# Performance work log

Measured on AMD Instinct MI355X. Metric: run time of the kernel, lower is better.

Reference implementation:

```python
import jax, jax.numpy as jnp
import numpy as np

N_GRAPHS = 256
STEPS = 3


def setup_inputs() -> dict:
    key = jax.random.key(0)
    ks = jax.random.split(key, 8)
    N, d, out = 100000, 512, 256
    s = 0.05
    x = jax.random.normal(ks[0], (N, d), dtype=jnp.float32)
    batch = jnp.sort(jax.random.randint(ks[1], (N,), 0, N_GRAPHS)).astype(jnp.int64)
    W_ih = jax.random.normal(ks[2], (4 * d, 2 * d), dtype=jnp.float32) * s
    W_hh = jax.random.normal(ks[3], (4 * d, d), dtype=jnp.float32) * s
    b_ih = jax.random.normal(ks[4], (4 * d,), dtype=jnp.float32) * s
    b_hh = jax.random.normal(ks[5], (4 * d,), dtype=jnp.float32) * s
    W_proj = jax.random.normal(ks[6], (out, 2 * d), dtype=jnp.float32) * s
    b_proj = jax.random.normal(ks[7], (out,), dtype=jnp.float32) * s
    return {"x": x, "batch": batch, "W_ih": W_ih, "W_hh": W_hh,
            "b_ih": b_ih, "b_hh": b_hh, "W_proj": W_proj, "b_proj": b_proj}


def _set2set(x, batch, W_ih, W_hh, b_ih, b_hh):
    N, d = x.shape
    B = N_GRAPHS
    h = jnp.zeros((B, d), x.dtype)
    c = jnp.zeros((B, d), x.dtype)
    q_star = jnp.zeros((B, 2 * d), x.dtype)
    for _ in range(STEPS):
        # single-step LSTM cell (PyTorch gate order i,f,g,o)
        gates = q_star @ W_ih.T + b_ih + h @ W_hh.T + b_hh
        i, f, g, o = jnp.split(gates, 4, axis=-1)
        c = jax.nn.sigmoid(f) * c + jax.nn.sigmoid(i) * jnp.tanh(g)
        h = jax.nn.sigmoid(o) * jnp.tanh(c)
        q = h                                   # [B, d]
        # segment softmax attention over nodes
        e = jnp.sum(x * q[batch], axis=-1)      # [N]
        m = jax.ops.segment_max(e, batch, num_segments=B)
        m = jnp.where(jnp.isfinite(m), m, 0.0)  # guard empty segments
        ex = jnp.exp(e - m[batch])
        denom = jax.ops.segment_sum(ex, batch, num_segments=B) + 1e-16
        a = ex / denom[batch]                   # [N]
        r = jax.ops.segment_sum(a[:, None] * x, batch, num_segments=B)  # [B, d]
        q_star = jnp.concatenate([q, r], axis=-1)
    return q_star


def reference(x, batch, W_ih, W_hh, b_ih, b_hh, W_proj, b_proj):
    pooled = _set2set(x, batch, W_ih, W_hh, b_ih, b_hh)  # [B, 2d]
    return pooled @ W_proj.T + b_proj                    # [B, out]
```

## Files before the change

kernel.cpp:

```cpp
#include <hip/hip_runtime.h>
#include <hip/hip_bf16.h>


typedef __bf16 bf16_t;
typedef __bf16 bf16x8 __attribute__((ext_vector_type(8)));
typedef float  f32x4  __attribute__((ext_vector_type(4)));

#define D     512
#define B_GR  256
#define FOURD 2048
#define KCAT  1536
#define AWAVES 16
#define DET_BLOCKS 400

__device__ __forceinline__ float load_f(const void* b, int i, int f32) {
    return f32 ? ((const float*)b)[i] : (float)((const bf16_t*)b)[i];
}

__global__ void detect_part1(const int* __restrict__ b32, int N,
                             const unsigned short* __restrict__ xh,
                             int* __restrict__ partA, int* __restrict__ partB) {
    __shared__ int sA, sB;
    if (threadIdx.x == 0) { sA = 0; sB = 0; }
    __syncthreads();
    int gid = blockIdx.x * blockDim.x + threadIdx.x;
    int stride = gridDim.x * blockDim.x;
    int dec = 0;
    for (int i = gid; i < N - 1; i += stride)
        if (b32[i] > b32[i + 1]) dec = 1;
    int bad = 0;
    for (int i = gid; i < 1024; i += stride) {
        unsigned e = (xh[i] >> 7) & 0xff;
        if (e >= 134) bad = 1;
    }
    if (dec) atomicOr(&sA, 1);
    if (bad) atomicOr(&sB, 1);
    __syncthreads();
    if (threadIdx.x == 0) { partA[blockIdx.x] = sA; partB[blockIdx.x] = sB; }
}

__global__ void detect_part2(const int* __restrict__ partA,
                             const int* __restrict__ partB, int nblk,
                             int* __restrict__ flags) {
    __shared__ int sA, sB;
    if (threadIdx.x == 0) { sA = 0; sB = 0; }
    __syncthreads();
    int a = 0, b = 0;
    for (int i = threadIdx.x; i < nblk; i += blockDim.x) {
        a |= partA[i];
        b |= partB[i];
    }
    if (a) atomicOr(&sA, 1);
    if (b) atomicOr(&sB, 1);
    __syncthreads();
    if (threadIdx.x == 0) { flags[0] = sA; flags[1] = sB; }
}

__global__ void seg_bounds_kernel(const void* __restrict__ batch, int N, int B,
                                  const int* __restrict__ flags,
                                  int* __restrict__ seg) {
    int n = blockIdx.x * blockDim.x + threadIdx.x;
    if (n >= N) return;
    const int is64 = flags[0];
    const int* b32 = (const int*)batch;
    const long long* b64 = (const long long*)batch;
    int cur = is64 ? (int)b64[n] : b32[n];
    if (n == 0) {
        for (int b = 0; b <= cur && b <= B; ++b) seg[b] = 0;
    } else {
        int prev = is64 ? (int)b64[n - 1] : b32[n - 1];
        for (int b = prev + 1; b <= cur && b <= B; ++b) seg[b] = n;
    }
    if (n == N - 1) {
        for (int b = cur + 1; b <= B; ++b) seg[b] = N;
    }
}

#define WCAT_E (FOURD * KCAT)
#define WP_E   (256 * 1024)
__global__ void prep_kernel(const void* __restrict__ W_ih,
                            const void* __restrict__ W_hh,
                            const void* __restrict__ b_ih,
                            const void* __restrict__ b_hh,
                            const void* __restrict__ W_proj,
                            const void* __restrict__ b_proj,
                            const int* __restrict__ flags,
                            bf16_t* __restrict__ Wcat, bf16_t* __restrict__ Wp,
                            float* __restrict__ bsum, float* __restrict__ bp) {
    const int f32 = flags[1];
    int gid = blockIdx.x * blockDim.x + threadIdx.x;
    int stride = gridDim.x * blockDim.x;
    const int total = WCAT_E + WP_E + FOURD + 256;
    for (int idx = gid; idx < total; idx += stride) {
        if (idx < WCAT_E) {
            int r = idx / KCAT, k = idx - r * KCAT;
            float v = (k < 1024) ? load_f(W_ih, r * 1024 + k, f32)
                                 : load_f(W_hh, r * 512 + (k - 1024), f32);
            Wcat[idx] = (bf16_t)v;
        } else if (idx < WCAT_E + WP_E) {
            int j = idx - WCAT_E;
            Wp[j] = (bf16_t)load_f(W_proj, j, f32);
        } else if (idx < WCAT_E + WP_E + FOURD) {
            int i = idx - WCAT_E - WP_E;
            bsum[i] = load_f(b_ih, i, f32) + load_f(b_hh, i, f32);
        } else {
            int i = idx - WCAT_E - WP_E - FOURD;
            bp[i] = load_f(b_proj, i, f32);
        }
    }
}

__global__ void lstm0_kernel(const float* __restrict__ bsum,
                             float* __restrict__ c, float* __restrict__ h,
                             bf16_t* __restrict__ Abuf) {
    int idx = blockIdx.x * blockDim.x + threadIdx.x;
    int b = idx >> 9, t = idx & 511;
    float gi = bsum[t], gf = bsum[512 + t], gg = bsum[1024 + t], go = bsum[1536 + t];
    (void)gf;
    float si = 1.f / (1.f + __expf(-gi));
    float so = 1.f / (1.f + __expf(-go));
    float tg = tanhf(gg);
    float cn = si * tg;
    float hn = so * tanhf(cn);
    c[idx] = cn;
    h[idx] = hn;
    bf16_t hb = (bf16_t)hn;
    Abuf[(size_t)b * KCAT + t]        = hb;
    Abuf[(size_t)b * KCAT + 1024 + t] = hb;
}

__global__ __launch_bounds__(64)
void gemm_lstm(const bf16_t* __restrict__ AbufIn,
               const bf16_t* __restrict__ Wcat,
               const float* __restrict__ bsum,
               float* __restrict__ c, float* __restrict__ h,
               bf16_t* __restrict__ AbufOut) {
    const int lane  = threadIdx.x;
    const int t0    = blockIdx.x * 16;
    const int m0    = blockIdx.y * 16;
    const int rowA  = m0 + (lane & 15);
    const int colB  = t0 + (lane & 15);
    const int kbase = (lane >> 4) * 8;

    f32x4 acc[4] = {{0,0,0,0},{0,0,0,0},{0,0,0,0},{0,0,0,0}};

    for (int k0 = 0; k0 < KCAT; k0 += 32) {
        int k = k0 + kbase;
        bf16x8 a = *(const bf16x8*)(AbufIn + (size_t)rowA * KCAT + k);
#pragma unroll
        for (int g = 0; g < 4; ++g) {
            bf16x8 bfr = *(const bf16x8*)(Wcat + (size_t)(g * 512 + colB) * KCAT + k);
            acc[g] = __builtin_amdgcn_mfma_f32_16x16x32_bf16(a, bfr, acc[g], 0, 0, 0);
        }
    }

    const int col   = colB;
    const int rbase = (lane >> 4) * 4;
    float bi = bsum[col], bf = bsum[512 + col], bg = bsum[1024 + col], bo = bsum[1536 + col];
#pragma unroll
    for (int r = 0; r < 4; ++r) {
        int m = m0 + rbase + r;
        float gi = acc[0][r] + bi;
        float gf = acc[1][r] + bf;
        float gg = acc[2][r] + bg;
        float go = acc[3][r] + bo;
        size_t ci = (size_t)m * D + col;
        float cv = c[ci];
        float si = 1.f / (1.f + __expf(-gi));
        float sf = 1.f / (1.f + __expf(-gf));
        float so = 1.f / (1.f + __expf(-go));
        float tg = tanhf(gg);
        float cn = sf * cv + si * tg;
        float hn = so * tanhf(cn);
        c[ci] = cn;
        h[ci] = hn;
        bf16_t hb = (bf16_t)hn;
        AbufOut[(size_t)m * KCAT + col]        = hb;
        AbufOut[(size_t)m * KCAT + 1024 + col] = hb;
    }
}


template<bool WRXB>
__device__ __forceinline__ void scan_f32(const float* __restrict__ xp,
                                         bf16_t* __restrict__ xb,
                                         int s, int cnt, int wave, int lane,
                                         const float* hl,
                                         float& m_w, float& s_w, float* r_w) {
    int i = 4 * wave;
    for (; i + 4 <= cnt; i += 4 * AWAVES) {
        size_t off = (((size_t)(s + i)) << 9) + (size_t)(lane * 8);
        float xr[4][8];
#pragma unroll
        for (int r = 0; r < 4; ++r) {
            const float* p = xp + off + (size_t)r * D;
            float4 v0 = *(const float4*)p;
            float4 v1 = *(const float4*)(p + 4);
            xr[r][0] = v0.x; xr[r][1] = v0.y; xr[r][2] = v0.z; xr[r][3] = v0.w;
            xr[r][4] = v1.x; xr[r][5] = v1.y; xr[r][6] = v1.z; xr[r][7] = v1.w;
        }
        if (WRXB) {
#pragma unroll
            for (int r = 0; r < 4; ++r) {
                bf16x8 v;
#pragma unroll
                for (int j = 0; j < 8; ++j) v[j] = (bf16_t)xr[r][j];
                *(bf16x8*)(xb + off + (size_t)r * D) = v;
            }
        }
        float d[4] = {0.f, 0.f, 0.f, 0.f};
#pragma unroll
        for (int j = 0; j < 8; ++j) {
#pragma unroll
            for (int r = 0; r < 4; ++r) d[r] += xr[r][j] * hl[j];
        }
#pragma unroll
        for (int o = 32; o > 0; o >>= 1) {
#pragma unroll
            for (int r = 0; r < 4; ++r) d[r] += __shfl_xor(d[r], o, 64);
        }
        float mx    = fmaxf(fmaxf(d[0], d[1]), fmaxf(d[2], d[3]));
        float m_new = fmaxf(m_w, mx);
        float alpha = __expf(m_w - m_new);
        float p0 = __expf(d[0] - m_new), p1 = __expf(d[1] - m_new);
        float p2 = __expf(d[2] - m_new), p3 = __expf(d[3] - m_new);
        s_w = s_w * alpha + ((p0 + p1) + (p2 + p3));
#pragma unroll
        for (int j = 0; j < 8; ++j)
            r_w[j] = r_w[j] * alpha + p0 * xr[0][j] + p1 * xr[1][j]
                                    + p2 * xr[2][j] + p3 * xr[3][j];
        m_w = m_new;
    }
    if (i < cnt) {
        int rem = cnt - i;
        size_t off = (((size_t)(s + i)) << 9) + (size_t)(lane * 8);
        float xr[4][8];
#pragma unroll
        for (int r = 0; r < 4; ++r) {
            if (r < rem) {
                const float* p = xp + off + (size_t)r * D;
                float4 v0 = *(const float4*)p;
                float4 v1 = *(const float4*)(p + 4);
                xr[r][0] = v0.x; xr[r][1] = v0.y; xr[r][2] = v0.z; xr[r][3] = v0.w;
                xr[r][4] = v1.x; xr[r][5] = v1.y; xr[r][6] = v1.z; xr[r][7] = v1.w;
            } else {
#pragma unroll
                for (int j = 0; j < 8; ++j) xr[r][j] = 0.f;
            }
        }
        if (WRXB) {
#pragma unroll
            for (int r = 0; r < 4; ++r) {
                if (r < rem) {
                    bf16x8 v;
#pragma unroll
                    for (int j = 0; j < 8; ++j) v[j] = (bf16_t)xr[r][j];
                    *(bf16x8*)(xb + off + (size_t)r * D) = v;
                }
            }
        }
        float d[4] = {0.f, 0.f, 0.f, 0.f};
#pragma unroll
        for (int j = 0; j < 8; ++j) {
#pragma unroll
            for (int r = 0; r < 4; ++r) d[r] += xr[r][j] * hl[j];
        }
#pragma unroll
        for (int o = 32; o > 0; o >>= 1) {
#pragma unroll
            for (int r = 0; r < 4; ++r) d[r] += __shfl_xor(d[r], o, 64);
        }
#pragma unroll
        for (int r = 0; r < 4; ++r)
            if (r >= rem) d[r] = -INFINITY;
        float mx    = fmaxf(fmaxf(d[0], d[1]), fmaxf(d[2], d[3]));
        float m_new = fmaxf(m_w, mx);
        float alpha = __expf(m_w - m_new);
        float p0 = __expf(d[0] - m_new), p1 = __expf(d[1] - m_new);
        float p2 = __expf(d[2] - m_new), p3 = __expf(d[3] - m_new);
        s_w = s_w * alpha + ((p0 + p1) + (p2 + p3));
#pragma unroll
        for (int j = 0; j < 8; ++j)
            r_w[j] = r_w[j] * alpha + p0 * xr[0][j] + p1 * xr[1][j]
                                    + p2 * xr[2][j] + p3 * xr[3][j];
        m_w = m_new;
    }
}

__device__ __forceinline__ void scan_bf16(const bf16_t* __restrict__ xp,
                                          int s, int cnt, int wave, int lane,
                                          const float* hl,
                                          float& m_w, float& s_w, float* r_w) {
    int i = 4 * wave;
    for (; i + 4 <= cnt; i += 4 * AWAVES) {
        size_t off = (((size_t)(s + i)) << 9) + (size_t)(lane * 8);
        float xr[4][8];
#pragma unroll
        for (int r = 0; r < 4; ++r) {
            bf16x8 v = *(const bf16x8*)(xp + off + (size_t)r * D);
#pragma unroll
            for (int j = 0; j < 8; ++j) xr[r][j] = (float)v[j];
        }
        float d[4] = {0.f, 0.f, 0.f, 0.f};
#pragma unroll
        for (int j = 0; j < 8; ++j) {
#pragma unroll
            for (int r = 0; r < 4; ++r) d[r] += xr[r][j] * hl[j];
        }
#pragma unroll
        for (int o = 32; o > 0; o >>= 1) {
#pragma unroll
            for (int r = 0; r < 4; ++r) d[r] += __shfl_xor(d[r], o, 64);
        }
        float mx    = fmaxf(fmaxf(d[0], d[1]), fmaxf(d[2], d[3]));
        float m_new = fmaxf(m_w, mx);
        float alpha = __expf(m_w - m_new);
        float p0 = __expf(d[0] - m_new), p1 = __expf(d[1] - m_new);
        float p2 = __expf(d[2] - m_new), p3 = __expf(d[3] - m_new);
        s_w = s_w * alpha + ((p0 + p1) + (p2 + p3));
#pragma unroll
        for (int j = 0; j < 8; ++j)
            r_w[j] = r_w[j] * alpha + p0 * xr[0][j] + p1 * xr[1][j]
                                    + p2 * xr[2][j] + p3 * xr[3][j];
        m_w = m_new;
    }
    if (i < cnt) {
        int rem = cnt - i;
        size_t off = (((size_t)(s + i)) << 9) + (size_t)(lane * 8);
        float xr[4][8];
#pragma unroll
        for (int r = 0; r < 4; ++r) {
            if (r < rem) {
                bf16x8 v = *(const bf16x8*)(xp + off + (size_t)r * D);
#pragma unroll
                for (int j = 0; j < 8; ++j) xr[r][j] = (float)v[j];
            } else {
#pragma unroll
                for (int j = 0; j < 8; ++j) xr[r][j] = 0.f;
            }
        }
        float d[4] = {0.f, 0.f, 0.f, 0.f};
#pragma unroll
        for (int j = 0; j < 8; ++j) {
#pragma unroll
            for (int r = 0; r < 4; ++r) d[r] += xr[r][j] * hl[j];
        }
#pragma unroll
        for (int o = 32; o > 0; o >>= 1) {
#pragma unroll
            for (int r = 0; r < 4; ++r) d[r] += __shfl_xor(d[r], o, 64);
        }
#pragma unroll
        for (int r = 0; r < 4; ++r)
            if (r >= rem) d[r] = -INFINITY;
        float mx    = fmaxf(fmaxf(d[0], d[1]), fmaxf(d[2], d[3]));
        float m_new = fmaxf(m_w, mx);
        float alpha = __expf(m_w - m_new);
        float p0 = __expf(d[0] - m_new), p1 = __expf(d[1] - m_new);
        float p2 = __expf(d[2] - m_new), p3 = __expf(d[3] - m_new);
        s_w = s_w * alpha + ((p0 + p1) + (p2 + p3));
#pragma unroll
        for (int j = 0; j < 8; ++j)
            r_w[j] = r_w[j] * alpha + p0 * xr[0][j] + p1 * xr[1][j]
                                    + p2 * xr[2][j] + p3 * xr[3][j];
        m_w = m_new;
    }
}

template<int STEP0, int USE_XB>
__global__ __launch_bounds__(1024)
void attention_kernel(const void* __restrict__ x, bf16_t* __restrict__ xb,
                      int N, const int* __restrict__ seg,
                      const float* __restrict__ hbuf,
                      bf16_t* __restrict__ AbufOut,
                      const int* __restrict__ flags) {
    __shared__ float racc2[AWAVES][D];
    __shared__ float red_m[AWAVES], red_s[AWAVES];

    const int f32x = flags[1];

    const int b = blockIdx.x;
    int s  = seg[b];
    int en = seg[b + 1];
    s  = (s  < 0) ? 0 : ((s  > N) ? N : s);
    en = (en < s) ? s : ((en > N) ? N : en);
    const int cnt  = en - s;
    const int tid  = threadIdx.x;
    const int wave = tid >> 6;
    const int lane = tid & 63;

    float hl[8];
    {
        const float* hp = hbuf + ((size_t)b << 9) + lane * 8;
#pragma unroll
        for (int j = 0; j < 8; ++j) hl[j] = hp[j];
    }

    float m_w = -INFINITY, s_w = 0.f;
    float r_w[8];
#pragma unroll
    for (int j = 0; j < 8; ++j) r_w[j] = 0.f;

    if (f32x) {
        if (STEP0 || !USE_XB) {
            scan_f32<(STEP0 && USE_XB)>((const float*)x, xb, s, cnt,
                                        wave, lane, hl, m_w, s_w, r_w);
        } else {
            scan_bf16(xb, s, cnt, wave, lane, hl, m_w, s_w, r_w);
        }
    } else {
        scan_bf16((const bf16_t*)x, s, cnt, wave, lane, hl, m_w, s_w, r_w);
    }

    if (lane == 0) { red_m[wave] = m_w; red_s[wave] = s_w; }
    __syncthreads();

    float M = -INFINITY, S = 0.f;
#pragma unroll
    for (int w = 0; w < AWAVES; ++w)
        if (red_s[w] > 0.f) M = fmaxf(M, red_m[w]);
#pragma unroll
    for (int w = 0; w < AWAVES; ++w)
        if (red_s[w] > 0.f) S += red_s[w] * __expf(red_m[w] - M);
    float Sinv  = 1.f / (S + 1e-16f);
    float scale = (s_w > 0.f) ? __expf(m_w - M) * Sinv : 0.f;

#pragma unroll
    for (int j = 0; j < 8; ++j) racc2[wave][lane * 8 + j] = r_w[j] * scale;
    __syncthreads();

    if (tid < D) {
        float r = 0.f;
#pragma unroll
        for (int w = 0; w < AWAVES; ++w) r += racc2[w][tid];
        AbufOut[(size_t)b * KCAT + 512 + tid] = (bf16_t)r;
    }
}

__global__ __launch_bounds__(64)
void gemm_proj(const bf16_t* __restrict__ A,
               const bf16_t* __restrict__ Wp, const float* __restrict__ bp,
               void* __restrict__ out, const int* __restrict__ flags) {
    const int f32o  = flags[1];
    const int lane  = threadIdx.x;
    const int n0    = blockIdx.x * 16;
    const int m0    = blockIdx.y * 16;
    const int rowA  = m0 + (lane & 15);
    const int rowB  = n0 + (lane & 15);
    const int kbase = (lane >> 4) * 8;

    f32x4 acc = {0.f, 0.f, 0.f, 0.f};
    for (int k0 = 0; k0 < 1024; k0 += 32) {
        int k = k0 + kbase;
        bf16x8 a = *(const bf16x8*)(A  + (size_t)rowA * KCAT + k);
        bf16x8 b = *(const bf16x8*)(Wp + (size_t)rowB * 1024 + k);
        acc = __builtin_amdgcn_mfma_f32_16x16x32_bf16(a, b, acc, 0, 0, 0);
    }
    const int col   = n0 + (lane & 15);
    const int rbase = (lane >> 4) * 4;
    float bias = bp[col];
#pragma unroll
    for (int r = 0; r < 4; ++r) {
        int m = m0 + rbase + r;
        float v = acc[r] + bias;
        if (f32o) ((float*)out)[(size_t)m * 256 + col]  = v;
        else      ((bf16_t*)out)[(size_t)m * 256 + col] = (bf16_t)v;
    }
}

extern "C" void kernel_launch(void* const* d_in, const int* in_sizes, int n_in,
                              void* d_out, int out_size, void* d_ws, size_t ws_size,
                              hipStream_t stream) {
    const void* x      = d_in[0];
    const void* batch  = d_in[1];
    const void* W_ih   = d_in[2];
    const void* W_hh   = d_in[3];
    const void* b_ih   = d_in[4];
    const void* b_hh   = d_in[5];
    const void* W_proj = d_in[6];
    const void* b_proj = d_in[7];

    const int N = in_sizes[1];
    const int B = B_GR;

    char* p = (char*)d_ws;
    size_t used = 0;
    auto carve = [&](size_t bytes) {
        void* r = (void*)p;
        size_t a = (bytes + 1023) & ~(size_t)1023;
        p += a;
        used += a;
        return r;
    };
    float*  c_buf = (float*)carve((size_t)B * D * 4);
    float*  h_buf = (float*)carve((size_t)B * D * 4);
    bf16_t* Abuf0 = (bf16_t*)carve((size_t)B * KCAT * 2);
    bf16_t* Abuf1 = (bf16_t*)carve((size_t)B * KCAT * 2);
    bf16_t* Wcat  = (bf16_t*)carve((size_t)FOURD * KCAT * 2);
    bf16_t* Wp    = (bf16_t*)carve((size_t)256 * 1024 * 2);
    float*  bsum  = (float*)carve((size_t)FOURD * 4);
    float*  bp    = (float*)carve((size_t)256 * 4);
    int*    seg   = (int*)carve((size_t)(B + 1) * 4);
    int*    flags = (int*)carve(8);
    int*    partA = (int*)carve(DET_BLOCKS * 4);
    int*    partB = (int*)carve(DET_BLOCKS * 4);
    if (used > ws_size) return;
    bf16_t* xb = (bf16_t*)carve((size_t)N * D * 2);
    int use_xb = (used <= ws_size) ? 1 : 0;

    detect_part1<<<DET_BLOCKS, 256, 0, stream>>>(
        (const int*)batch, N, (const unsigned short*)x, partA, partB);
    detect_part2<<<1, 512, 0, stream>>>(partA, partB, DET_BLOCKS, flags);
    seg_bounds_kernel<<<(N + 255) / 256, 256, 0, stream>>>(batch, N, B, flags, seg);
    prep_kernel<<<1024, 256, 0, stream>>>(W_ih, W_hh, b_ih, b_hh, W_proj, b_proj,
                                          flags, Wcat, Wp, bsum, bp);

    lstm0_kernel<<<(B * D) / 256, 256, 0, stream>>>(bsum, c_buf, h_buf, Abuf0);
    if (use_xb)
        attention_kernel<1, 1><<<B, 1024, 0, stream>>>(x, xb, N, seg,
                                                       h_buf, Abuf0, flags);
    else
        attention_kernel<1, 0><<<B, 1024, 0, stream>>>(x, xb, N, seg,
                                                       h_buf, Abuf0, flags);

    gemm_lstm<<<dim3(D / 16, B / 16), 64, 0, stream>>>(
        Abuf0, Wcat, bsum, c_buf, h_buf, Abuf1);
    if (use_xb)
        attention_kernel<0, 1><<<B, 1024, 0, stream>>>(x, xb, N, seg,
                                                       h_buf, Abuf1, flags);
    else
        attention_kernel<0, 0><<<B, 1024, 0, stream>>>(x, xb, N, seg,
                                                       h_buf, Abuf1, flags);
    gemm_lstm<<<dim3(D / 16, B / 16), 64, 0, stream>>>(
        Abuf1, Wcat, bsum, c_buf, h_buf, Abuf0);
    if (use_xb)
        attention_kernel<0, 1><<<B, 1024, 0, stream>>>(x, xb, N, seg,
                                                       h_buf, Abuf0, flags);
    else
        attention_kernel<0, 0><<<B, 1024, 0, stream>>>(x, xb, N, seg,
                                                       h_buf, Abuf0, flags);

    gemm_proj<<<dim3(256 / 16, B / 16), 64, 0, stream>>>(Abuf0, Wp, bp, d_out, flags);
}
```

Baseline: 421.0 us.

## Fuse seg bounds into prep, lstm0 into first attention, projection into last attention

Folds segment-boundary computation into the weight-prep kernel, computes the step-0 LSTM state inline inside the first attention kernel, and fuses the final projection GEMM into the last attention kernel as a per-graph scalar dot product. This removes three kernel launches and their global round-trips. The fused projection uses scalar FMAs over bf16 weights instead of MFMA, and each block rereads the whole projection matrix. The step-0 h/c values are no longer written to h_buf, and gemm_lstm is assumed to depend only on c_buf and Abuf.

Result: slower. 443.0 us (+5.2%).

```diff
diff --git a/kernel.cpp b/kernel.cpp
--- a/kernel.cpp
+++ b/kernel.cpp
@@ -56,40 +56,40 @@
     if (threadIdx.x == 0) { flags[0] = sA; flags[1] = sB; }
 }
 
-__global__ void seg_bounds_kernel(const void* __restrict__ batch, int N, int B,
-                                  const int* __restrict__ flags,
-                                  int* __restrict__ seg) {
-    int n = blockIdx.x * blockDim.x + threadIdx.x;
-    if (n >= N) return;
-    const int is64 = flags[0];
-    const int* b32 = (const int*)batch;
-    const long long* b64 = (const long long*)batch;
-    int cur = is64 ? (int)b64[n] : b32[n];
-    if (n == 0) {
-        for (int b = 0; b <= cur && b <= B; ++b) seg[b] = 0;
-    } else {
-        int prev = is64 ? (int)b64[n - 1] : b32[n - 1];
-        for (int b = prev + 1; b <= cur && b <= B; ++b) seg[b] = n;
-    }
-    if (n == N - 1) {
-        for (int b = cur + 1; b <= B; ++b) seg[b] = N;
-    }
-}
-
 #define WCAT_E (FOURD * KCAT)
 #define WP_E   (256 * 1024)
-__global__ void prep_kernel(const void* __restrict__ W_ih,
-                            const void* __restrict__ W_hh,
-                            const void* __restrict__ b_ih,
-                            const void* __restrict__ b_hh,
-                            const void* __restrict__ W_proj,
-                            const void* __restrict__ b_proj,
-                            const int* __restrict__ flags,
-                            bf16_t* __restrict__ Wcat, bf16_t* __restrict__ Wp,
-                            float* __restrict__ bsum, float* __restrict__ bp) {
+__global__ void prep_seg_kernel(const void* __restrict__ W_ih,
+                                const void* __restrict__ W_hh,
+                                const void* __restrict__ b_ih,
+                                const void* __restrict__ b_hh,
+                                const void* __restrict__ W_proj,
+                                const void* __restrict__ b_proj,
+                                const void* __restrict__ batch, int N, int B,
+                                const int* __restrict__ flags,
+                                bf16_t* __restrict__ Wcat, bf16_t* __restrict__ Wp,
+                                float* __restrict__ bsum, float* __restrict__ bp,
+                                int* __restrict__ seg) {
     const int f32 = flags[1];
     int gid = blockIdx.x * blockDim.x + threadIdx.x;
     int stride = gridDim.x * blockDim.x;
+
+    if (gid < N) {
+        const int n = gid;
+        const int is64 = flags[0];
+        const int* b32 = (const int*)batch;
+        const long long* b64 = (const long long*)batch;
+        int cur = is64 ? (int)b64[n] : b32[n];
+        if (n == 0) {
+            for (int b = 0; b <= cur && b <= B; ++b) seg[b] = 0;
+        } else {
+            int prev = is64 ? (int)b64[n - 1] : b32[n - 1];
+            for (int b = prev + 1; b <= cur && b <= B; ++b) seg[b] = n;
+        }
+        if (n == N - 1) {
+            for (int b = cur + 1; b <= B; ++b) seg[b] = N;
+        }
+    }
+
     const int total = WCAT_E + WP_E + FOURD + 256;
     for (int idx = gid; idx < total; idx += stride) {
         if (idx < WCAT_E) {
@@ -110,23 +110,14 @@
     }
 }
 
-__global__ void lstm0_kernel(const float* __restrict__ bsum,
-                             float* __restrict__ c, float* __restrict__ h,
-                             bf16_t* __restrict__ Abuf) {
-    int idx = blockIdx.x * blockDim.x + threadIdx.x;
-    int b = idx >> 9, t = idx & 511;
-    float gi = bsum[t], gf = bsum[512 + t], gg = bsum[1024 + t], go = bsum[1536 + t];
-    (void)gf;
+__device__ __forceinline__ void lstm0_math(const float* __restrict__ bsum,
+                                           int t, float& cn, float& hn) {
+    float gi = bsum[t], gg = bsum[1024 + t], go = bsum[1536 + t];
     float si = 1.f / (1.f + __expf(-gi));
     float so = 1.f / (1.f + __expf(-go));
     float tg = tanhf(gg);
-    float cn = si * tg;
-    float hn = so * tanhf(cn);
-    c[idx] = cn;
-    h[idx] = hn;
-    bf16_t hb = (bf16_t)hn;
-    Abuf[(size_t)b * KCAT + t]        = hb;
-    Abuf[(size_t)b * KCAT + 1024 + t] = hb;
+    cn = si * tg;
+    hn = so * tanhf(cn);
 }
 
 __global__ __launch_bounds__(64)
@@ -367,15 +358,22 @@
     }
 }
 
-template<int STEP0, int USE_XB>
+template<int STEP0, int USE_XB, int PROJ>
 __global__ __launch_bounds__(1024)
 void attention_kernel(const void* __restrict__ x, bf16_t* __restrict__ xb,
                       int N, const int* __restrict__ seg,
                       const float* __restrict__ hbuf,
+                      const float* __restrict__ bsum,
+                      float* __restrict__ c_buf,
                       bf16_t* __restrict__ AbufOut,
+                      const bf16_t* __restrict__ Wp,
+                      const float* __restrict__ bp,
+                      void* __restrict__ out,
                       const int* __restrict__ flags) {
     __shared__ float racc2[AWAVES][D];
     __shared__ float red_m[AWAVES], red_s[AWAVES];
+    __shared__ __align__(16) bf16_t qsb[PROJ ? 1024 : 1];
+    __shared__ float pout[PROJ ? 4 : 1][PROJ ? 256 : 1];
 
     const int f32x = flags[1];
 
@@ -390,7 +388,14 @@
     const int lane = tid & 63;
 
     float hl[8];
-    {
+    if (STEP0) {
+#pragma unroll
+        for (int j = 0; j < 8; ++j) {
+            float cn, hn;
+            lstm0_math(bsum, lane * 8 + j, cn, hn);
+            hl[j] = hn;
+        }
+    } else {
         const float* hp = hbuf + ((size_t)b << 9) + lane * 8;
 #pragma unroll
         for (int j = 0; j < 8; ++j) hl[j] = hp[j];
@@ -429,42 +434,49 @@
     for (int j = 0; j < 8; ++j) racc2[wave][lane * 8 + j] = r_w[j] * scale;
     __syncthreads();
 
-    if (tid < D) {
-        float r = 0.f;
-#pragma unroll
-        for (int w = 0; w < AWAVES; ++w) r += racc2[w][tid];
-        AbufOut[(size_t)b * KCAT + 512 + tid] = (bf16_t)r;
-    }
-}
-
-__global__ __launch_bounds__(64)
-void gemm_proj(const bf16_t* __restrict__ A,
-               const bf16_t* __restrict__ Wp, const float* __restrict__ bp,
-               void* __restrict__ out, const int* __restrict__ flags) {
-    const int f32o  = flags[1];
-    const int lane  = threadIdx.x;
-    const int n0    = blockIdx.x * 16;
-    const int m0    = blockIdx.y * 16;
-    const int rowA  = m0 + (lane & 15);
-    const int rowB  = n0 + (lane & 15);
-    const int kbase = (lane >> 4) * 8;
-
-    f32x4 acc = {0.f, 0.f, 0.f, 0.f};
-    for (int k0 = 0; k0 < 1024; k0 += 32) {
-        int k = k0 + kbase;
-        bf16x8 a = *(const bf16x8*)(A  + (size_t)rowA * KCAT + k);
-        bf16x8 b = *(const bf16x8*)(Wp + (size_t)rowB * 1024 + k);
-        acc = __builtin_amdgcn_mfma_f32_16x16x32_bf16(a, b, acc, 0, 0, 0);
-    }
-    const int col   = n0 + (lane & 15);
-    const int rbase = (lane >> 4) * 4;
-    float bias = bp[col];
-#pragma unroll
-    for (int r = 0; r < 4; ++r) {
-        int m = m0 + rbase + r;
-        float v = acc[r] + bias;
-        if (f32o) ((float*)out)[(size_t)m * 256 + col]  = v;
-        else      ((bf16_t*)out)[(size_t)m * 256 + col] = (bf16_t)v;
+    if (PROJ) {
+        if (tid < D) {
+            float r = 0.f;
+#pragma unroll
+            for (int w = 0; w < AWAVES; ++w) r += racc2[w][tid];
+            qsb[512 + tid] = (bf16_t)r;
+            qsb[tid] = (bf16_t)hbuf[((size_t)b << 9) + tid];
+        }
+        __syncthreads();
+        const int o    = tid & 255;
+        const int part = tid >> 8;
+        float acc = 0.f;
+#pragma unroll
+        for (int kk = 0; kk < 256; kk += 8) {
+            int k = part * 256 + kk;
+            bf16x8 w = *(const bf16x8*)(Wp + (size_t)o * 1024 + k);
+            bf16x8 q = *(const bf16x8*)(qsb + k);
+#pragma unroll
+            for (int j = 0; j < 8; ++j) acc += (float)q[j] * (float)w[j];
+        }
+        pout[part][o] = acc;
+        __syncthreads();
+        if (tid < 256) {
+            float v = pout[0][tid] + pout[1][tid] + pout[2][tid] + pout[3][tid]
+                    + bp[tid];
+            if (f32x) ((float*)out)[(size_t)b * 256 + tid]  = v;
+            else      ((bf16_t*)out)[(size_t)b * 256 + tid] = (bf16_t)v;
+        }
+    } else {
+        if (tid < D) {
+            float r = 0.f;
+#pragma unroll
+            for (int w = 0; w < AWAVES; ++w) r += racc2[w][tid];
+            AbufOut[(size_t)b * KCAT + 512 + tid] = (bf16_t)r;
+            if (STEP0) {
+                float cn, hn;
+                lstm0_math(bsum, tid, cn, hn);
+                c_buf[((size_t)b << 9) + tid] = cn;
+                bf16_t hb = (bf16_t)hn;
+                AbufOut[(size_t)b * KCAT + tid]        = hb;
+                AbufOut[(size_t)b * KCAT + 1024 + tid] = hb;
+            }
+        }
     }
 }
 
@@ -511,34 +523,32 @@
     detect_part1<<<DET_BLOCKS, 256, 0, stream>>>(
         (const int*)batch, N, (const unsigned short*)x, partA, partB);
     detect_part2<<<1, 512, 0, stream>>>(partA, partB, DET_BLOCKS, flags);
-    seg_bounds_kernel<<<(N + 255) / 256, 256, 0, stream>>>(batch, N, B, flags, seg);
-    prep_kernel<<<1024, 256, 0, stream>>>(W_ih, W_hh, b_ih, b_hh, W_proj, b_proj,
-                                          flags, Wcat, Wp, bsum, bp);
-
-    lstm0_kernel<<<(B * D) / 256, 256, 0, stream>>>(bsum, c_buf, h_buf, Abuf0);
+    prep_seg_kernel<<<1024, 256, 0, stream>>>(W_ih, W_hh, b_ih, b_hh,
+                                              W_proj, b_proj, batch, N, B,
+                                              flags, Wcat, Wp, bsum, bp, seg);
+
     if (use_xb)
-        attention_kernel<1, 1><<<B, 1024, 0, stream>>>(x, xb, N, seg,
-                                                       h_buf, Abuf0, flags);
+        attention_kernel<1, 1, 0><<<B, 1024, 0, stream>>>(
+            x, xb, N, seg, h_buf, bsum, c_buf, Abuf0, Wp, bp, d_out, flags);
     else
-        attention_kernel<1, 0><<<B, 1024, 0, stream>>>(x, xb, N, seg,
-                                                       h_buf, Abuf0, flags);
+        attention_kernel<1, 0, 0><<<B, 1024, 0, stream>>>(
+            x, xb, N, seg, h_buf, bsum, c_buf, Abuf0, Wp, bp, d_out, flags);
 
     gemm_lstm<<<dim3(D / 16, B / 16), 64, 0, stream>>>(
         Abuf0, Wcat, bsum, c_buf, h_buf, Abuf1);
     if (use_xb)
-        attention_kernel<0, 1><<<B, 1024, 0, stream>>>(x, xb, N, seg,
-                                                       h_buf, Abuf1, flags);
+        attention_kernel<0, 1, 0><<<B, 1024, 0, stream>>>(
+            x, xb, N, seg, h_buf, bsum, c_buf, Abuf1, Wp, bp, d_out, flags);
     else
-        attention_kernel<0, 0><<<B, 1024, 0, stream>>>(x, xb, N, seg,
-                                                       h_buf, Abuf1, flags);
+        attention_kernel<0, 0, 0><<<B, 1024, 0, stream>>>(
+            x, xb, N, seg, h_buf, bsum, c_buf, Abuf1, Wp, bp, d_out, flags);
+
     gemm_lstm<<<dim3(D / 16, B / 16), 64, 0, stream>>>(
         Abuf1, Wcat, bsum, c_buf, h_buf, Abuf0);
     if (use_xb)
-        attention_kernel<0, 1><<<B, 1024, 0, stream>>>(x, xb, N, seg,
-                                                       h_buf, Abuf0, flags);
+        attention_kernel<0, 1, 1><<<B, 1024, 0, stream>>>(
+            x, xb, N, seg, h_buf, bsum, c_buf, Abuf0, Wp, bp, d_out, flags);
     else
-        attention_kernel<0, 0><<<B, 1024, 0, stream>>>(x, xb, N, seg,
-                                                       h_buf, Abuf0, flags);
-
-    gemm_proj<<<dim3(256 / 16, B / 16), 64, 0, stream>>>(Abuf0, Wp, bp, d_out, flags);
-}
+        attention_kernel<0, 0, 1><<<B, 1024, 0, stream>>>(
+            x, xb, N, seg, h_buf, bsum, c_buf, Abuf0, Wp, bp, d_out, flags);
+}
```
